# Optimization experiments

Measured on AMD Instinct MI355X. Metric: run time of the kernel, lower is better.

## Reference

```python
import jax, jax.numpy as jnp
import numpy as np

N = 16384
L = 4096  # n_locations

def setup_inputs() -> dict:
    key = jax.random.key(0)
    k1, k2, k3, k4 = jax.random.split(key, 4)
    w = jax.random.randint(k1, (N,), 0, L)
    z = jax.random.normal(k2, (N, L), dtype=jnp.float32)
    W = jax.random.normal(k3, (L, L), dtype=jnp.float32) * (1.0 / np.sqrt(L))
    b = jax.random.normal(k4, (L,), dtype=jnp.float32) * 0.01
    return {"w": w, "z": z, "W": W, "b": b}

def reference(w, z, W, b):
    # zw[i] = z[i, w[i]]
    zw = jnp.take_along_axis(z, w[:, None], axis=1)[:, 0]  # [N]
    # Original: inp = scatter(zw at column w); out = inp @ W.T + b
    # Mathematically: out[i, j] = zw[i] * W[j, w[i]] + b[j]
    out = zw[:, None] * W.T[w] + b  # [N, L]
    return out
```

## Files before the change

### kernel.cpp

```cpp
#include <hip/hip_runtime.h>

#define N_ROWS 16384
#define L_DIM  4096
#define CG     32
#define JT     256
#define NBKT   (L_DIM / CG)
#define NJT    (L_DIM / JT)
#define PITCH  (JT + 4)
#define CAP    512

__global__ __launch_bounds__(256, 4) void pnet_fused(
    const int* __restrict__ w,
    const float* __restrict__ z,
    const float* __restrict__ W,
    const float* __restrict__ b,
    float* __restrict__ out)
{
    __shared__ float tile[CG * PITCH];
    __shared__ int   list[CAP];
    __shared__ float zlist[CAP];
    __shared__ int   cnt;

    const int tid  = threadIdx.x;
    const int l0   = blockIdx.x * CG;
    const int j0   = blockIdx.y * JT;
    const int wid  = tid >> 6;
    const int lane = tid & 63;

    if (tid == 0) cnt = 0;

    const float4 bbv = *(const float4*)&b[j0 + lane * 4];

    __syncthreads();

    {
        const int q     = tid & 7;
        const int rbase = tid >> 3;
        #pragma unroll
        for (int it = 0; it < JT / 32; ++it) {
            const int r = rbase + it * 32;
            const float4 v = *(const float4*)&W[(size_t)(j0 + r) * L_DIM + l0 + 4 * q];
            tile[(4 * q + 0) * PITCH + r] = v.x;
            tile[(4 * q + 1) * PITCH + r] = v.y;
            tile[(4 * q + 2) * PITCH + r] = v.z;
            tile[(4 * q + 3) * PITCH + r] = v.w;
        }
    }

    #pragma unroll
    for (int s = 0; s < N_ROWS / 1024; ++s) {
        const int i0  = s * 1024 + tid * 4;
        const int4 wv = *(const int4*)&w[i0];
        const int vals[4] = {wv.x, wv.y, wv.z, wv.w};
        #pragma unroll
        for (int e = 0; e < 4; ++e) {
            const unsigned c = (unsigned)(vals[e] - l0);
            if (c < CG) {
                const int pos = atomicAdd(&cnt, 1);
                if (pos < CAP) list[pos] = (i0 + e) | ((int)c << 16);
            }
        }
    }

    __syncthreads();
    const int n     = cnt;
    const int nmain = n < CAP ? n : CAP;

    for (int e = tid; e < nmain; e += 256) {
        const int ent = list[e];
        zlist[e] = z[(unsigned)((ent & 0xFFFF) * L_DIM) + (unsigned)(ent >> 16) + l0];
    }
    __syncthreads();

    for (int e = wid; e < nmain; e += 4) {
        const int   ent = list[e];
        const int   i   = ent & 0xFFFF;
        const int   c   = ent >> 16;
        const float zw  = zlist[e];
        const float4 wv4 = *(const float4*)&tile[c * PITCH + lane * 4];
        float4 o;
        o.x = fmaf(zw, wv4.x, bbv.x);
        o.y = fmaf(zw, wv4.y, bbv.y);
        o.z = fmaf(zw, wv4.z, bbv.z);
        o.w = fmaf(zw, wv4.w, bbv.w);
        *(float4*)&out[(unsigned)(i * L_DIM) + j0 + lane * 4] = o;
    }

    if (n > CAP) {
        for (int p = 0; p < N_ROWS / 512; ++p) {
            __syncthreads();
            if (tid == 0) cnt = 0;
            __syncthreads();
            const int i0  = p * 512 + tid * 2;
            const int2 wv = *(const int2*)&w[i0];
            const int vals[2] = {wv.x, wv.y};
            #pragma unroll
            for (int e = 0; e < 2; ++e) {
                const unsigned c = (unsigned)(vals[e] - l0);
                if (c < CG) {
                    const int pos = atomicAdd(&cnt, 1);
                    list[pos]  = (i0 + e) | ((int)c << 16);
                    zlist[pos] = z[(unsigned)((i0 + e) * L_DIM) + vals[e]];
                }
            }
            __syncthreads();
            const int np = cnt;
            for (int e = wid; e < np; e += 4) {
                const int   ent = list[e];
                const int   i   = ent & 0xFFFF;
                const int   c   = ent >> 16;
                const float zw  = zlist[e];
                const float4 wv4 = *(const float4*)&tile[c * PITCH + lane * 4];
                float4 o;
                o.x = fmaf(zw, wv4.x, bbv.x);
                o.y = fmaf(zw, wv4.y, bbv.y);
                o.z = fmaf(zw, wv4.z, bbv.z);
                o.w = fmaf(zw, wv4.w, bbv.w);
                *(float4*)&out[(unsigned)(i * L_DIM) + j0 + lane * 4] = o;
            }
        }
    }
}

extern "C" void kernel_launch(void* const* d_in, const int* in_sizes, int n_in,
                              void* d_out, int out_size, void* d_ws, size_t ws_size,
                              hipStream_t stream) {
    const int*   w = (const int*)d_in[0];
    const float* z = (const float*)d_in[1];
    const float* W = (const float*)d_in[2];
    const float* b = (const float*)d_in[3];
    float* out = (float*)d_out;

    dim3 grid(NBKT, NJT);
    pnet_fused<<<grid, 256, 0, stream>>>(w, z, W, b, out);
}
```

Baseline: 81.73 us.

## Halve location group, widen column tile with double-buffered W chunks

Each block now handles 16 locations and 1024 output columns, processed as four 256-column chunks. The next W chunk is staged into a second shared buffer while the current one is consumed, and W loads and output stores use nontemporal hints. This cuts how often each block rescans w, since the w scan is now amortised over more columns, and overlaps W staging with output writes. The cost is more registers for bias values, an extra barrier per chunk and a larger shared footprint. Grid shape changes from 128x16 to 256x4 blocks.

```diff
diff --git a/kernel.cpp b/kernel.cpp
--- a/kernel.cpp
+++ b/kernel.cpp
@@ -2,12 +2,14 @@
 
 #define N_ROWS 16384
 #define L_DIM  4096
-#define CG     32
-#define JT     256
-#define NBKT   (L_DIM / CG)
-#define NJT    (L_DIM / JT)
-#define PITCH  (JT + 4)
+#define CG     16
+#define JT     1024
+#define CHUNK  256
+#define NCHUNK (JT / CHUNK)
+#define PITCH  (CHUNK + 4)
 #define CAP    512
+
+typedef float f32x4 __attribute__((ext_vector_type(4)));
 
 __global__ __launch_bounds__(256, 4) void pnet_fused(
     const int* __restrict__ w,
@@ -16,7 +18,7 @@
     const float* __restrict__ b,
     float* __restrict__ out)
 {
-    __shared__ float tile[CG * PITCH];
+    __shared__ float tile[2][CG * PITCH];
     __shared__ int   list[CAP];
     __shared__ float zlist[CAP];
     __shared__ int   cnt;
@@ -29,25 +31,14 @@
 
     if (tid == 0) cnt = 0;
 
-    const float4 bbv = *(const float4*)&b[j0 + lane * 4];
+    f32x4 bb[NCHUNK];
+    #pragma unroll
+    for (int cc = 0; cc < NCHUNK; ++cc)
+        bb[cc] = *(const f32x4*)&b[j0 + cc * CHUNK + lane * 4];
 
     __syncthreads();
 
-    {
-        const int q     = tid & 7;
-        const int rbase = tid >> 3;
-        #pragma unroll
-        for (int it = 0; it < JT / 32; ++it) {
-            const int r = rbase + it * 32;
-            const float4 v = *(const float4*)&W[(size_t)(j0 + r) * L_DIM + l0 + 4 * q];
-            tile[(4 * q + 0) * PITCH + r] = v.x;
-            tile[(4 * q + 1) * PITCH + r] = v.y;
-            tile[(4 * q + 2) * PITCH + r] = v.z;
-            tile[(4 * q + 3) * PITCH + r] = v.w;
-        }
-    }
-
-    #pragma unroll
+    #pragma unroll 4
     for (int s = 0; s < N_ROWS / 1024; ++s) {
         const int i0  = s * 1024 + tid * 4;
         const int4 wv = *(const int4*)&w[i0];
@@ -61,7 +52,6 @@
             }
         }
     }
-
     __syncthreads();
     const int n     = cnt;
     const int nmain = n < CAP ? n : CAP;
@@ -70,28 +60,53 @@
         const int ent = list[e];
         zlist[e] = z[(unsigned)((ent & 0xFFFF) * L_DIM) + (unsigned)(ent >> 16) + l0];
     }
+
+#define STAGE(cc, buf)                                                              \
+    {                                                                               \
+        const int q     = tid & 3;                                                  \
+        const int rbase = tid >> 2;                                                 \
+        _Pragma("unroll")                                                           \
+        for (int it = 0; it < CHUNK / 64; ++it) {                                   \
+            const int r = rbase + it * 64;                                          \
+            const f32x4 v = __builtin_nontemporal_load(                             \
+                (const f32x4*)&W[(size_t)(j0 + (cc) * CHUNK + r) * L_DIM + l0 + 4 * q]); \
+            tile[buf][(4 * q + 0) * PITCH + r] = v.x;                               \
+            tile[buf][(4 * q + 1) * PITCH + r] = v.y;                               \
+            tile[buf][(4 * q + 2) * PITCH + r] = v.z;                               \
+            tile[buf][(4 * q + 3) * PITCH + r] = v.w;                               \
+        }                                                                           \
+    }
+
+    STAGE(0, 0);
     __syncthreads();
 
-    for (int e = wid; e < nmain; e += 4) {
-        const int   ent = list[e];
-        const int   i   = ent & 0xFFFF;
-        const int   c   = ent >> 16;
-        const float zw  = zlist[e];
-        const float4 wv4 = *(const float4*)&tile[c * PITCH + lane * 4];
-        float4 o;
-        o.x = fmaf(zw, wv4.x, bbv.x);
-        o.y = fmaf(zw, wv4.y, bbv.y);
-        o.z = fmaf(zw, wv4.z, bbv.z);
-        o.w = fmaf(zw, wv4.w, bbv.w);
-        *(float4*)&out[(unsigned)(i * L_DIM) + j0 + lane * 4] = o;
+    for (int cc = 0; cc < NCHUNK; ++cc) {
+        const int cur = cc & 1;
+        if (cc + 1 < NCHUNK) STAGE(cc + 1, cur ^ 1);
+
+        for (int e = wid; e < nmain; e += 4) {
+            const int   ent = list[e];
+            const int   i   = ent & 0xFFFF;
+            const int   c   = ent >> 16;
+            const float zw  = zlist[e];
+            const f32x4 wv4 = *(const f32x4*)&tile[cur][c * PITCH + lane * 4];
+            f32x4 o;
+            o.x = fmaf(zw, wv4.x, bb[cc].x);
+            o.y = fmaf(zw, wv4.y, bb[cc].y);
+            o.z = fmaf(zw, wv4.z, bb[cc].z);
+            o.w = fmaf(zw, wv4.w, bb[cc].w);
+            __builtin_nontemporal_store(o,
+                (f32x4*)&out[(unsigned)(i * L_DIM) + j0 + cc * CHUNK + lane * 4]);
+        }
+        __syncthreads();
     }
 
     if (n > CAP) {
-        for (int p = 0; p < N_ROWS / 512; ++p) {
+        for (int p = 0; p < N_ROWS / CAP; ++p) {
             __syncthreads();
             if (tid == 0) cnt = 0;
             __syncthreads();
-            const int i0  = p * 512 + tid * 2;
+            const int i0  = p * CAP + tid * 2;
             const int2 wv = *(const int2*)&w[i0];
             const int vals[2] = {wv.x, wv.y};
             #pragma unroll
@@ -105,21 +120,27 @@
             }
             __syncthreads();
             const int np = cnt;
-            for (int e = wid; e < np; e += 4) {
-                const int   ent = list[e];
-                const int   i   = ent & 0xFFFF;
-                const int   c   = ent >> 16;
-                const float zw  = zlist[e];
-                const float4 wv4 = *(const float4*)&tile[c * PITCH + lane * 4];
-                float4 o;
-                o.x = fmaf(zw, wv4.x, bbv.x);
-                o.y = fmaf(zw, wv4.y, bbv.y);
-                o.z = fmaf(zw, wv4.z, bbv.z);
-                o.w = fmaf(zw, wv4.w, bbv.w);
-                *(float4*)&out[(unsigned)(i * L_DIM) + j0 + lane * 4] = o;
+            for (int cc = 0; cc < NCHUNK; ++cc) {
+                STAGE(cc, 0);
+                __syncthreads();
+                for (int e = wid; e < np; e += 4) {
+                    const int   ent = list[e];
+                    const int   i   = ent & 0xFFFF;
+                    const int   c   = ent >> 16;
+                    const float zw  = zlist[e];
+                    const f32x4 wv4 = *(const f32x4*)&tile[0][c * PITCH + lane * 4];
+                    f32x4 o;
+                    o.x = fmaf(zw, wv4.x, bb[cc].x);
+                    o.y = fmaf(zw, wv4.y, bb[cc].y);
+                    o.z = fmaf(zw, wv4.z, bb[cc].z);
+                    o.w = fmaf(zw, wv4.w, bb[cc].w);
+                    *(f32x4*)&out[(unsigned)(i * L_DIM) + j0 + cc * CHUNK + lane * 4] = o;
+                }
+                __syncthreads();
             }
         }
     }
+#undef STAGE
 }
 
 extern "C" void kernel_launch(void* const* d_in, const int* in_sizes, int n_in,
@@ -131,6 +152,6 @@
     const float* b = (const float*)d_in[3];
     float* out = (float*)d_out;
 
-    dim3 grid(NBKT, NJT);
+    dim3 grid(L_DIM / CG, L_DIM / JT);
     pnet_fused<<<grid, 256, 0, stream>>>(w, z, W, b, out);
 }
```

Result: slower. 101.6 us (+24.3%).

## Persist blocks over column phases with double-buffered W tiles and prefetch

Applied to the files above, without the earlier changes.

Reorganizes the grid so each block owns 16 locations and half of the output columns, looping over four 512-wide column phases. The W tile for the next phase is prefetched into registers and written to a second LDS buffer while the current phase is stored. This amortizes the w-scan bucketing over more output and overlaps W loads with output stores. Output stores and W loads become nontemporal. The grid drops from 2048 to 512 blocks with lower occupancy bounds, so there is less parallelism and more register pressure, and the overflow path is rewritten.

```diff
diff --git a/kernel.cpp b/kernel.cpp
--- a/kernel.cpp
+++ b/kernel.cpp
@@ -2,50 +2,64 @@
 
 #define N_ROWS 16384
 #define L_DIM  4096
-#define CG     32
-#define JT     256
-#define NBKT   (L_DIM / CG)
-#define NJT    (L_DIM / JT)
+#define CG     16
+#define JT     512
+#define NPH    4
 #define PITCH  (JT + 4)
-#define CAP    512
+#define CAP    384
 
-__global__ __launch_bounds__(256, 4) void pnet_fused(
+typedef float f32x4 __attribute__((ext_vector_type(4)));
+
+__global__ __launch_bounds__(256, 2) void pnet_fused(
     const int* __restrict__ w,
     const float* __restrict__ z,
     const float* __restrict__ W,
     const float* __restrict__ b,
     float* __restrict__ out)
 {
-    __shared__ float tile[CG * PITCH];
+    __shared__ float tile[2][CG * PITCH];
     __shared__ int   list[CAP];
     __shared__ float zlist[CAP];
     __shared__ int   cnt;
 
-    const int tid  = threadIdx.x;
-    const int l0   = blockIdx.x * CG;
-    const int j0   = blockIdx.y * JT;
-    const int wid  = tid >> 6;
-    const int lane = tid & 63;
+    const int tid   = threadIdx.x;
+    const int g     = blockIdx.x >> 1;
+    const int half  = blockIdx.x & 1;
+    const int l0    = g * CG;
+    const int jh    = half * (NPH * JT);
+    const int wid   = tid >> 6;
+    const int lane  = tid & 63;
+    const int q     = tid & 3;
+    const int rbase = tid >> 2;
 
     if (tid == 0) cnt = 0;
 
-    const float4 bbv = *(const float4*)&b[j0 + lane * 4];
+    f32x4 pf[8];
 
-    __syncthreads();
+#define PF_ISSUE(t)                                                            \
+    {                                                                          \
+        _Pragma("unroll")                                                      \
+        for (int it = 0; it < 8; ++it) {                                       \
+            const int r = rbase + it * 64;                                     \
+            pf[it] = __builtin_nontemporal_load((const f32x4*)                 \
+                &W[(size_t)(jh + (t) * JT + r) * L_DIM + l0 + 4 * q]);         \
+        }                                                                      \
+    }
 
-    {
-        const int q     = tid & 7;
-        const int rbase = tid >> 3;
-        #pragma unroll
-        for (int it = 0; it < JT / 32; ++it) {
-            const int r = rbase + it * 32;
-            const float4 v = *(const float4*)&W[(size_t)(j0 + r) * L_DIM + l0 + 4 * q];
-            tile[(4 * q + 0) * PITCH + r] = v.x;
-            tile[(4 * q + 1) * PITCH + r] = v.y;
-            tile[(4 * q + 2) * PITCH + r] = v.z;
-            tile[(4 * q + 3) * PITCH + r] = v.w;
-        }
+#define DSWRITE(buf)                                                           \
+    {                                                                          \
+        _Pragma("unroll")                                                      \
+        for (int it = 0; it < 8; ++it) {                                       \
+            const int r = rbase + it * 64;                                     \
+            tile[buf][(4 * q + 0) * PITCH + r] = pf[it].x;                     \
+            tile[buf][(4 * q + 1) * PITCH + r] = pf[it].y;                     \
+            tile[buf][(4 * q + 2) * PITCH + r] = pf[it].z;                     \
+            tile[buf][(4 * q + 3) * PITCH + r] = pf[it].w;                     \
+        }                                                                      \
     }
+
+    PF_ISSUE(0);
+    __builtin_amdgcn_sched_barrier(0);
 
     #pragma unroll
     for (int s = 0; s < N_ROWS / 1024; ++s) {
@@ -61,65 +75,105 @@
             }
         }
     }
-
     __syncthreads();
     const int n     = cnt;
     const int nmain = n < CAP ? n : CAP;
 
-    for (int e = tid; e < nmain; e += 256) {
-        const int ent = list[e];
-        zlist[e] = z[(unsigned)((ent & 0xFFFF) * L_DIM) + (unsigned)(ent >> 16) + l0];
-    }
-    __syncthreads();
+    if (n <= CAP) {
+        for (int e = tid; e < nmain; e += 256) {
+            const int ent = list[e];
+            zlist[e] = z[(unsigned)((ent & 0xFFFF) * L_DIM) + (unsigned)(ent >> 16) + l0];
+        }
+        DSWRITE(0);
+        __syncthreads();
 
-    for (int e = wid; e < nmain; e += 4) {
-        const int   ent = list[e];
-        const int   i   = ent & 0xFFFF;
-        const int   c   = ent >> 16;
-        const float zw  = zlist[e];
-        const float4 wv4 = *(const float4*)&tile[c * PITCH + lane * 4];
-        float4 o;
-        o.x = fmaf(zw, wv4.x, bbv.x);
-        o.y = fmaf(zw, wv4.y, bbv.y);
-        o.z = fmaf(zw, wv4.z, bbv.z);
-        o.w = fmaf(zw, wv4.w, bbv.w);
-        *(float4*)&out[(unsigned)(i * L_DIM) + j0 + lane * 4] = o;
-    }
+        for (int t = 0; t < NPH; ++t) {
+            const int cur = t & 1;
+            if (t + 1 < NPH) {
+                PF_ISSUE(t + 1);
+                __builtin_amdgcn_sched_barrier(0);
+            }
+            const int j0 = jh + t * JT;
+            const f32x4 bv0 = *(const f32x4*)&b[j0 + lane * 4];
+            const f32x4 bv1 = *(const f32x4*)&b[j0 + lane * 4 + 256];
 
-    if (n > CAP) {
-        for (int p = 0; p < N_ROWS / 512; ++p) {
-            __syncthreads();
-            if (tid == 0) cnt = 0;
-            __syncthreads();
-            const int i0  = p * 512 + tid * 2;
-            const int2 wv = *(const int2*)&w[i0];
-            const int vals[2] = {wv.x, wv.y};
-            #pragma unroll
-            for (int e = 0; e < 2; ++e) {
-                const unsigned c = (unsigned)(vals[e] - l0);
-                if (c < CG) {
-                    const int pos = atomicAdd(&cnt, 1);
-                    list[pos]  = (i0 + e) | ((int)c << 16);
-                    zlist[pos] = z[(unsigned)((i0 + e) * L_DIM) + vals[e]];
-                }
-            }
-            __syncthreads();
-            const int np = cnt;
-            for (int e = wid; e < np; e += 4) {
+            for (int e = wid; e < nmain; e += 4) {
                 const int   ent = list[e];
                 const int   i   = ent & 0xFFFF;
                 const int   c   = ent >> 16;
                 const float zw  = zlist[e];
-                const float4 wv4 = *(const float4*)&tile[c * PITCH + lane * 4];
-                float4 o;
-                o.x = fmaf(zw, wv4.x, bbv.x);
-                o.y = fmaf(zw, wv4.y, bbv.y);
-                o.z = fmaf(zw, wv4.z, bbv.z);
-                o.w = fmaf(zw, wv4.w, bbv.w);
-                *(float4*)&out[(unsigned)(i * L_DIM) + j0 + lane * 4] = o;
+                const f32x4 w0  = *(const f32x4*)&tile[cur][c * PITCH + lane * 4];
+                const f32x4 w1  = *(const f32x4*)&tile[cur][c * PITCH + lane * 4 + 256];
+                f32x4 o0, o1;
+                o0.x = fmaf(zw, w0.x, bv0.x);
+                o0.y = fmaf(zw, w0.y, bv0.y);
+                o0.z = fmaf(zw, w0.z, bv0.z);
+                o0.w = fmaf(zw, w0.w, bv0.w);
+                o1.x = fmaf(zw, w1.x, bv1.x);
+                o1.y = fmaf(zw, w1.y, bv1.y);
+                o1.z = fmaf(zw, w1.z, bv1.z);
+                o1.w = fmaf(zw, w1.w, bv1.w);
+                const unsigned base = (unsigned)(i * L_DIM) + j0 + lane * 4;
+                __builtin_nontemporal_store(o0, (f32x4*)&out[base]);
+                __builtin_nontemporal_store(o1, (f32x4*)&out[base + 256]);
+            }
+            __syncthreads();
+            if (t + 1 < NPH) {
+                DSWRITE(cur ^ 1);
+                __syncthreads();
+            }
+        }
+    } else {
+        DSWRITE(0);
+        for (int t = 0; t < NPH; ++t) {
+            if (t > 0) {
+                __syncthreads();
+                PF_ISSUE(t);
+                DSWRITE(0);
+            }
+            __syncthreads();
+            const int j0 = jh + t * JT;
+            const f32x4 bv0 = *(const f32x4*)&b[j0 + lane * 4];
+            const f32x4 bv1 = *(const f32x4*)&b[j0 + lane * 4 + 256];
+            for (int base0 = 0; base0 < N_ROWS; base0 += 256) {
+                __syncthreads();
+                if (tid == 0) cnt = 0;
+                __syncthreads();
+                const int i  = base0 + tid;
+                const int wi = w[i];
+                const unsigned c = (unsigned)(wi - l0);
+                if (c < CG) {
+                    const int pos = atomicAdd(&cnt, 1);
+                    list[pos]  = i | ((int)c << 16);
+                    zlist[pos] = z[(size_t)i * L_DIM + wi];
+                }
+                __syncthreads();
+                const int np = cnt;
+                for (int e = wid; e < np; e += 4) {
+                    const int   ent = list[e];
+                    const int   ii  = ent & 0xFFFF;
+                    const int   c2  = ent >> 16;
+                    const float zw  = zlist[e];
+                    const f32x4 w0  = *(const f32x4*)&tile[0][c2 * PITCH + lane * 4];
+                    const f32x4 w1  = *(const f32x4*)&tile[0][c2 * PITCH + lane * 4 + 256];
+                    f32x4 o0, o1;
+                    o0.x = fmaf(zw, w0.x, bv0.x);
+                    o0.y = fmaf(zw, w0.y, bv0.y);
+                    o0.z = fmaf(zw, w0.z, bv0.z);
+                    o0.w = fmaf(zw, w0.w, bv0.w);
+                    o1.x = fmaf(zw, w1.x, bv1.x);
+                    o1.y = fmaf(zw, w1.y, bv1.y);
+                    o1.z = fmaf(zw, w1.z, bv1.z);
+                    o1.w = fmaf(zw, w1.w, bv1.w);
+                    const unsigned base = (unsigned)(ii * L_DIM) + j0 + lane * 4;
+                    *(f32x4*)&out[base]       = o0;
+                    *(f32x4*)&out[base + 256] = o1;
+                }
             }
         }
     }
+#undef PF_ISSUE
+#undef DSWRITE
 }
 
 extern "C" void kernel_launch(void* const* d_in, const int* in_sizes, int n_in,
@@ -131,6 +185,5 @@
     const float* b = (const float*)d_in[3];
     float* out = (float*)d_out;
 
-    dim3 grid(NBKT, NJT);
-    pnet_fused<<<grid, 256, 0, stream>>>(w, z, W, b, out);
+    pnet_fused<<<512, 256, 0, stream>>>(w, z, W, b, out);
 }
```

Result: slower. 98.48 us (+20.5%).
